# Kernel tuning notes

Hardware: AMD Instinct MI355X
Metric: run time of the kernel (lower is better)

Reference implementation:

```python
import jax, jax.numpy as jnp
import numpy as np
import math

D = 1024
H = 16

def _new_gelu(x):
    return 0.5 * x * (1.0 + jnp.tanh(math.sqrt(2.0 / math.pi) * (x + 0.044715 * x ** 3)))

def _layer_norm(x, w):
    mu = jnp.mean(x, axis=-1, keepdims=True)
    var = jnp.var(x, axis=-1, keepdims=True)
    return (x - mu) * jax.lax.rsqrt(var + 1e-5) * w

def setup_inputs() -> dict:
    key = jax.random.key(0)
    ks = jax.random.split(key, 8)
    B, T = 2, 2048
    s = lambda fan_in: 1.0 / math.sqrt(fan_in)
    return {
        "x": jax.random.normal(ks[0], (B, T, D), jnp.float32),
        "ln1_w": jnp.ones((D,), jnp.float32),
        "attn_w": jax.random.normal(ks[1], (D, 3 * D), jnp.float32) * s(D),
        "attn_b": jnp.zeros((3 * D,), jnp.float32),
        "proj_w": jax.random.normal(ks[2], (D, D), jnp.float32) * s(D),
        "proj_b": jnp.zeros((D,), jnp.float32),
        "ln2_w": jnp.ones((D,), jnp.float32),
        "li1_w": jax.random.normal(ks[3], (D, 4 * D), jnp.float32) * s(D),
        "li1_b": jnp.zeros((4 * D,), jnp.float32),
        "li2_w": jax.random.normal(ks[4], (4 * D, D), jnp.float32) * s(4 * D),
        "li2_b": jnp.zeros((D,), jnp.float32),
    }

def reference(x, ln1_w, attn_w, attn_b, proj_w, proj_b, ln2_w, li1_w, li1_b, li2_w, li2_b):
    B, T, C = x.shape
    Dh = C // H
    # --- causal self-attention on pre-LN input ---
    h = _layer_norm(x, ln1_w)
    qkv = h @ attn_w + attn_b                      # [B,T,3C]
    q, k, v = jnp.split(qkv, 3, axis=-1)
    q = q.reshape(B, T, H, Dh)
    k = k.reshape(B, T, H, Dh)
    v = v.reshape(B, T, H, Dh)
    # NOTE: faithful to source — scale is 1/sqrt(BATCH), not 1/sqrt(head_dim)
    scale = 1.0 / math.sqrt(B)
    scores = jnp.einsum('bthd,bshd->bhts', q, k) * scale   # [B,H,T,T]
    causal = jnp.tril(jnp.ones((T, T), bool))
    scores = jnp.where(causal, scores, -jnp.inf)
    attn = jax.nn.softmax(scores, axis=-1)
    o = jnp.einsum('bhts,bshd->bthd', attn, v).reshape(B, T, C)
    x = x + o @ proj_w + proj_b
    # --- MLP ---
    h = _layer_norm(x, ln2_w)
    x = x + _new_gelu(h @ li1_w + li1_b) @ li2_w + li2_b
    return x
```

## Files before the change

kernel.cpp:

```cpp
#include <hip/hip_runtime.h>

typedef _Float16 f16;
typedef _Float16 f16x8 __attribute__((ext_vector_type(8)));
typedef _Float16 f16x4 __attribute__((ext_vector_type(4)));
typedef float    f32x4 __attribute__((ext_vector_type(4)));
typedef float    f32x16 __attribute__((ext_vector_type(16)));
typedef unsigned u32;
typedef unsigned u32x4 __attribute__((ext_vector_type(4)));

#define GAS __attribute__((address_space(1)))
#define LAS __attribute__((address_space(3)))

static __device__ __forceinline__ void gload_lds16(const void* g, void* l) {
    __builtin_amdgcn_global_load_lds((const GAS void*)g, (LAS void*)l, 16, 0, 0);
}

__global__ void wconv_t(const float* __restrict__ w, f16* __restrict__ wt, int K, int N) {
    __shared__ f16 t[32][33];
    const int tx = threadIdx.x, ty = threadIdx.y;
    const int n0 = blockIdx.x * 32, k0 = blockIdx.y * 32;
#pragma unroll
    for (int i = 0; i < 4; i++)
        t[ty + i * 8][tx] = (f16)w[(size_t)(k0 + ty + i * 8) * N + n0 + tx];
    __syncthreads();
#pragma unroll
    for (int i = 0; i < 4; i++)
        wt[(size_t)(n0 + ty + i * 8) * K + k0 + tx] = t[tx][ty + i * 8];
}

__global__ __launch_bounds__(256) void ln_kernel(const float* __restrict__ x,
                                                 const float* __restrict__ w,
                                                 f16* __restrict__ h) {
    const int row = blockIdx.x, tid = threadIdx.x;
    const float4 v = reinterpret_cast<const float4*>(x)[(size_t)row * 256 + tid];
    float s = v.x + v.y + v.z + v.w;
    float q = v.x * v.x + v.y * v.y + v.z * v.z + v.w * v.w;
#pragma unroll
    for (int m = 1; m < 64; m <<= 1) { s += __shfl_xor(s, m); q += __shfl_xor(q, m); }
    __shared__ float ss[4], qq[4];
    if ((tid & 63) == 0) { ss[tid >> 6] = s; qq[tid >> 6] = q; }
    __syncthreads();
    s = ss[0] + ss[1] + ss[2] + ss[3];
    q = qq[0] + qq[1] + qq[2] + qq[3];
    const float mu = s * (1.0f / 1024.0f);
    const float var = q * (1.0f / 1024.0f) - mu * mu;
    const float rs = rsqrtf(var + 1e-5f);
    const float4 wv = reinterpret_cast<const float4*>(w)[tid];
    f16x4 o;
    o[0] = (f16)((v.x - mu) * rs * wv.x);
    o[1] = (f16)((v.y - mu) * rs * wv.y);
    o[2] = (f16)((v.z - mu) * rs * wv.z);
    o[3] = (f16)((v.w - mu) * rs * wv.w);
    reinterpret_cast<f16x4*>(h)[(size_t)row * 256 + tid] = o;
}

__global__ __launch_bounds__(256) void vtrans(const f16* __restrict__ V, f16* __restrict__ Vt) {
    __shared__ f16 tl[64][72];
    const int tid = threadIdx.x;
    const int t0 = blockIdx.x * 64, bh = blockIdx.y;
    const int b = bh >> 4, hh = bh & 15;
    const int rr = tid >> 3, cc = (tid & 7) * 8;
#pragma unroll
    for (int p = 0; p < 2; p++) {
        f16x8 v = *(const f16x8*)(V + (size_t)(b * 2048 + t0 + p * 32 + rr) * 1024 + hh * 64 + cc);
#pragma unroll
        for (int j = 0; j < 8; j++) tl[p * 32 + rr][cc + j] = v[j];
    }
    __syncthreads();
#pragma unroll
    for (int p = 0; p < 2; p++) {
        const int d = p * 32 + rr;
        f16x8 o;
#pragma unroll
        for (int j = 0; j < 8; j++) o[j] = tl[cc + j][d];
        *(f16x8*)(Vt + (size_t)(bh * 64 + d) * 2048 + t0 + cc) = o;
    }
}

template <int EPI>
__global__ __launch_bounds__(512) void gemm_f16(
    const f16* __restrict__ A, int lda,
    const f16* __restrict__ Bt, int ldb,
    const float* __restrict__ bias,
    const float* __restrict__ res,
    void* __restrict__ outp,
    f16* __restrict__ oq, f16* __restrict__ ok, f16* __restrict__ ov,
    int N, int K) {
    __shared__ alignas(16) f16 As[3][128 * 32];
    __shared__ alignas(16) f16 Bs[3][128 * 32];
    const int tid = threadIdx.x;
    const int lane = tid & 63, wv = tid >> 6;
    const int wr = wv >> 2, wc = wv & 3;
    const int m0 = blockIdx.x * 128, n0 = blockIdx.y * 128;
    const int l15 = lane & 15, lg = lane >> 4;

    f32x4 acc[4][2] = {};

    const int ar = tid >> 2;
    const int ac = (tid & 3) * 8;
    const size_t koff = (size_t)blockIdx.z * K;
    const f16* gA = A + (size_t)(m0 + ar) * lda + ac + koff;
    const f16* gB = Bt + (size_t)(n0 + ar) * ldb + ac + koff;
    char* lA0 = (char*)As + wv * 1024;
    char* lB0 = (char*)Bs + wv * 1024;

    auto stage = [&](int buf, int k0) {
        gload_lds16(gA + k0, lA0 + buf * 8192);
        gload_lds16(gB + k0, lB0 + buf * 8192);
    };
    auto compute = [&](int buf) {
        f16x8 af[4], bf[2];
#pragma unroll
        for (int i = 0; i < 4; i++)
            af[i] = *(const f16x8*)&As[buf][(wr * 64 + i * 16 + l15) * 32 + lg * 8];
#pragma unroll
        for (int n = 0; n < 2; n++)
            bf[n] = *(const f16x8*)&Bs[buf][(wc * 32 + n * 16 + l15) * 32 + lg * 8];
#pragma unroll
        for (int mi = 0; mi < 4; mi++)
#pragma unroll
            for (int ni = 0; ni < 2; ni++)
                acc[mi][ni] = __builtin_amdgcn_mfma_f32_16x16x32_f16(af[mi], bf[ni], acc[mi][ni], 0, 0, 0);
    };

    const int nk = K >> 5;
    stage(0, 0);
    if (nk > 1) {
        stage(1, 32);
        asm volatile("s_waitcnt vmcnt(2)" ::: "memory");
    } else {
        asm volatile("s_waitcnt vmcnt(0)" ::: "memory");
    }
    __builtin_amdgcn_s_barrier();

    for (int t = 0; t < nk; ++t) {
        const bool pref = (t + 2 < nk);
        if (pref) stage((t + 2) % 3, (t + 2) * 32);
        compute(t % 3);
        if (t + 1 < nk) {
            if (pref) asm volatile("s_waitcnt vmcnt(2)" ::: "memory");
            else      asm volatile("s_waitcnt vmcnt(0)" ::: "memory");
            __builtin_amdgcn_s_barrier();
        }
    }

#pragma unroll
    for (int mi = 0; mi < 4; mi++) {
#pragma unroll
        for (int ni = 0; ni < 2; ni++) {
            const int gc = n0 + wc * 32 + ni * 16 + l15;
            const float bb = (EPI == 3) ? 0.0f : bias[gc];
#pragma unroll
            for (int r = 0; r < 4; r++) {
                const int gr = m0 + wr * 64 + mi * 16 + lg * 4 + r;
                float v = acc[mi][ni][r] + bb;
                if (EPI == 0) {
                    if (gc < 1024)      oq[(size_t)gr * 1024 + gc]        = (f16)(v * 0.70710678118654752f);
                    else if (gc < 2048) ok[(size_t)gr * 1024 + gc - 1024] = (f16)v;
                    else                ov[(size_t)gr * 1024 + gc - 2048] = (f16)v;
                } else if (EPI == 1) {
                    ((float*)outp)[(size_t)gr * N + gc] = v + res[(size_t)gr * N + gc];
                } else if (EPI == 2) {
                    const float z = 0.7978845608028654f * (v + 0.044715f * v * v * v);
                    const float t = 1.0f - 2.0f / (__builtin_amdgcn_exp2f(2.8853900817779268f * z) + 1.0f);
                    ((f16*)outp)[(size_t)gr * N + gc] = (f16)(0.5f * v * (1.0f + t));
                } else {
                    float* P = (float*)outp + (size_t)blockIdx.z * ((size_t)gridDim.x * 128) * N;
                    P[(size_t)gr * N + gc] = v;
                }
            }
        }
    }
}

__global__ __launch_bounds__(256) void kred(const float* __restrict__ p0,
                                            const float* __restrict__ p1,
                                            const float* __restrict__ bias,
                                            const float* __restrict__ res,
                                            float* __restrict__ out) {
    const size_t i = (size_t)blockIdx.x * 256 + threadIdx.x;
    const float4 a = ((const float4*)p0)[i];
    const float4 b = ((const float4*)p1)[i];
    const float4 r = ((const float4*)res)[i];
    const float4 w = ((const float4*)bias)[i & 255];
    float4 o;
    o.x = a.x + b.x + r.x + w.x;
    o.y = a.y + b.y + r.y + w.y;
    o.z = a.z + b.z + r.z + w.z;
    o.w = a.w + b.w + r.w + w.w;
    ((float4*)out)[i] = o;
}

__global__ __launch_bounds__(256, 2) void attn_kernel(
    const f16* __restrict__ Q, const f16* __restrict__ Kb,
    const f16* __restrict__ Vt, f16* __restrict__ O) {
    __shared__ f16 ot[4][32][72];
    const int tid = threadIdx.x, lane = tid & 63, w = tid >> 6;
    const int l31 = lane & 31, hi = lane >> 5;
    const int bx = blockIdx.x;
    const int bh = bx & 31, jj = bx >> 5;
    const int b = bh >> 4, hh = bh & 15;
    const int qtile = (15 - jj) * 4 + w;
    const int q0 = qtile * 32;

    const f16* qrow = Q + (size_t)(b * 2048 + q0 + l31) * 1024 + hh * 64 + hi * 8;
    f16x8 qf[4];
#pragma unroll
    for (int s = 0; s < 4; s++) qf[s] = *(const f16x8*)(qrow + s * 16);

    f32x16 oacc[2] = {};
    float m = -3e38f, l = 0.0f;

    const f16* kbase = Kb + (size_t)b * 2048 * 1024 + hh * 64 + hi * 8;
    const f16* vrow0 = Vt + (size_t)(bh * 64 + l31) * 2048 + hi * 8;
    const f16* vrow1 = vrow0 + (size_t)32 * 2048;

    const int nt = qtile + 1;

    f16x8 ka[4], va[4], kb2[4], vb2[4];
    auto loadKV = [&](int kt, f16x8* kf, f16x8* vf) {
        const f16* kr = kbase + (size_t)(kt * 32 + l31) * 1024;
#pragma unroll
        for (int s = 0; s < 4; s++) kf[s] = *(const f16x8*)(kr + s * 16);
        vf[0] = *(const f16x8*)(vrow0 + kt * 32);
        vf[1] = *(const f16x8*)(vrow0 + kt * 32 + 16);
        vf[2] = *(const f16x8*)(vrow1 + kt * 32);
        vf[3] = *(const f16x8*)(vrow1 + kt * 32 + 16);
    };

    auto tilestep = [&](const f16x8* kf, const f16x8* vf, bool diag) {
        f32x16 sacc = {};
        __builtin_amdgcn_s_setprio(1);
#pragma unroll
        for (int s = 0; s < 4; s++)
            sacc = __builtin_amdgcn_mfma_f32_32x32x16_f16(kf[s], qf[s], sacc, 0, 0, 0);
        __builtin_amdgcn_s_setprio(0);
        if (diag) {
#pragma unroll
            for (int r = 0; r < 16; r++) {
                const int key = (r & 3) + 8 * (r >> 2) + 4 * hi;
                sacc[r] = (key > l31) ? -3e38f : sacc[r];
            }
        }
        float t8[8];
#pragma unroll
        for (int i = 0; i < 8; i++) t8[i] = fmaxf(sacc[2 * i], sacc[2 * i + 1]);
#pragma unroll
        for (int i = 0; i < 4; i++) t8[i] = fmaxf(t8[i], t8[i + 4]);
        float tm = fmaxf(fmaxf(t8[0], t8[1]), fmaxf(t8[2], t8[3]));
        tm = fmaxf(tm, __shfl_xor(tm, 32));
        const bool up = tm > m + 8.0f;
        if (__any(up)) {
            const float mnew = up ? tm : m;
            const float alpha = __expf(m - mnew);
            m = mnew;
            l *= alpha;
#pragma unroll
            for (int r = 0; r < 16; r++) { oacc[0][r] *= alpha; oacc[1][r] *= alpha; }
        }
        const float mref = m * 1.44269504f;
        float p[16];
#pragma unroll
        for (int r = 0; r < 16; r++)
            p[r] = __builtin_amdgcn_exp2f(sacc[r] * 1.44269504f - mref);
        float s8[8];
#pragma unroll
        for (int i = 0; i < 8; i++) s8[i] = p[2 * i] + p[2 * i + 1];
#pragma unroll
        for (int i = 0; i < 4; i++) s8[i] = s8[i] + s8[i + 4];
        float psum = (s8[0] + s8[1]) + (s8[2] + s8[3]);
        psum += __shfl_xor(psum, 32);
        l += psum;

        u32 wd[8];
#pragma unroll
        for (int i = 0; i < 8; i++)
            wd[i] = __builtin_bit_cast(u32, __builtin_amdgcn_cvt_pkrtz(p[2 * i], p[2 * i + 1]));
        const u32 e0 = __shfl_xor(hi ? wd[0] : wd[2], 32);
        const u32 e1 = __shfl_xor(hi ? wd[1] : wd[3], 32);
        const u32 e2 = __shfl_xor(hi ? wd[4] : wd[6], 32);
        const u32 e3 = __shfl_xor(hi ? wd[5] : wd[7], 32);
        u32x4 b0, b1;
        b0[0] = hi ? e0 : wd[0]; b0[1] = hi ? e1 : wd[1];
        b0[2] = hi ? wd[2] : e0; b0[3] = hi ? wd[3] : e1;
        b1[0] = hi ? e2 : wd[4]; b1[1] = hi ? e3 : wd[5];
        b1[2] = hi ? wd[6] : e2; b1[3] = hi ? wd[7] : e3;
        const f16x8 pb0 = __builtin_bit_cast(f16x8, b0);
        const f16x8 pb1 = __builtin_bit_cast(f16x8, b1);

        __builtin_amdgcn_s_setprio(1);
        oacc[0] = __builtin_amdgcn_mfma_f32_32x32x16_f16(vf[0], pb0, oacc[0], 0, 0, 0);
        oacc[0] = __builtin_amdgcn_mfma_f32_32x32x16_f16(vf[1], pb1, oacc[0], 0, 0, 0);
        oacc[1] = __builtin_amdgcn_mfma_f32_32x32x16_f16(vf[2], pb0, oacc[1], 0, 0, 0);
        oacc[1] = __builtin_amdgcn_mfma_f32_32x32x16_f16(vf[3], pb1, oacc[1], 0, 0, 0);
        __builtin_amdgcn_s_setprio(0);
    };

    loadKV(0, ka, va);
    int kt = 0;
    for (; kt + 2 <= nt; kt += 2) {
        loadKV(kt + 1, kb2, vb2);
        tilestep(ka, va, false);
        if (kt + 2 < nt) loadKV(kt + 2, ka, va);
        tilestep(kb2, vb2, (kt + 1) == qtile);
    }
    if (kt < nt) tilestep(ka, va, true);

    const float inv = 1.0f / l;
#pragma unroll
    for (int dt = 0; dt < 2; dt++)
#pragma unroll
        for (int r = 0; r < 16; r++) {
            const int d = dt * 32 + (r & 3) + 8 * (r >> 2) + 4 * hi;
            ot[w][l31][d] = (f16)(oacc[dt][r] * inv);
        }
    asm volatile("s_waitcnt lgkmcnt(0)" ::: "memory");
#pragma unroll
    for (int i = 0; i < 4; i++) {
        const int row = i * 8 + (lane >> 3), col = (lane & 7) * 8;
        const f16x8 o8 = *(const f16x8*)&ot[w][row][col];
        *(f16x8*)(O + (size_t)(b * 2048 + q0 + row) * 1024 + hh * 64 + col) = o8;
    }
}

extern "C" void kernel_launch(void* const* d_in, const int* in_sizes, int n_in,
                              void* d_out, int out_size, void* d_ws, size_t ws_size,
                              hipStream_t stream) {
    const float* x      = (const float*)d_in[0];
    const float* ln1_w  = (const float*)d_in[1];
    const float* attn_w = (const float*)d_in[2];
    const float* attn_b = (const float*)d_in[3];
    const float* proj_w = (const float*)d_in[4];
    const float* proj_b = (const float*)d_in[5];
    const float* ln2_w  = (const float*)d_in[6];
    const float* li1_w  = (const float*)d_in[7];
    const float* li1_b  = (const float*)d_in[8];
    const float* li2_w  = (const float*)d_in[9];
    const float* li2_b  = (const float*)d_in[10];
    float* out = (float*)d_out;

    char* ws = (char*)d_ws;
    size_t off = 0;
    auto alloc = [&](size_t bytes) { void* p = ws + off; off += (bytes + 255) & ~(size_t)255; return p; };
    f16* W1t = (f16*)alloc((size_t)3072 * 1024 * 2);
    f16* W2t = (f16*)alloc((size_t)1024 * 1024 * 2);
    f16* W3t = (f16*)alloc((size_t)4096 * 1024 * 2);
    f16* W4t = (f16*)alloc((size_t)1024 * 4096 * 2);
    f16* h   = (f16*)alloc((size_t)4096 * 1024 * 2);
    f16* Qb  = (f16*)alloc((size_t)4096 * 1024 * 2);
    f16* Kb  = (f16*)alloc((size_t)4096 * 1024 * 2);
    f16* Vb  = (f16*)alloc((size_t)4096 * 1024 * 2);
    f16* Vt  = (f16*)alloc((size_t)4096 * 1024 * 2);
    f16* Ob  = (f16*)alloc((size_t)4096 * 1024 * 2);
    float* x1 = (float*)alloc((size_t)4096 * 1024 * 4);
    float* P  = (float*)alloc((size_t)2 * 4096 * 1024 * 4);
    f16* Ab = Qb;

    dim3 b328(32, 8);
    wconv_t<<<dim3(96, 32),  b328, 0, stream>>>(attn_w, W1t, 1024, 3072);
    wconv_t<<<dim3(32, 32),  b328, 0, stream>>>(proj_w, W2t, 1024, 1024);
    wconv_t<<<dim3(128, 32), b328, 0, stream>>>(li1_w,  W3t, 1024, 4096);
    wconv_t<<<dim3(32, 128), b328, 0, stream>>>(li2_w,  W4t, 4096, 1024);

    ln_kernel<<<4096, 256, 0, stream>>>(x, ln1_w, h);
    gemm_f16<0><<<dim3(32, 24), 512, 0, stream>>>(h, 1024, W1t, 1024, attn_b, nullptr,
                                                  nullptr, Qb, Kb, Vb, 3072, 1024);
    vtrans<<<dim3(32, 32), 256, 0, stream>>>(Vb, Vt);
    attn_kernel<<<512, 256, 0, stream>>>(Qb, Kb, Vt, Ob);
    gemm_f16<1><<<dim3(32, 8), 512, 0, stream>>>(Ob, 1024, W2t, 1024, proj_b, x,
                                                 x1, nullptr, nullptr, nullptr, 1024, 1024);
    ln_kernel<<<4096, 256, 0, stream>>>(x1, ln2_w, h);
    gemm_f16<2><<<dim3(32, 32), 512, 0, stream>>>(h, 1024, W3t, 1024, li1_b, nullptr,
                                                  Ab, nullptr, nullptr, nullptr, 4096, 1024);
    gemm_f16<3><<<dim3(32, 8, 2), 512, 0, stream>>>(Ab, 4096, W4t, 4096, nullptr, nullptr,
                                                    P, nullptr, nullptr, nullptr, 1024, 2048);
    kred<<<4096, 256, 0, stream>>>(P, P + (size_t)4096 * 1024, li2_b, x1, out);
}
```

Measured before the change: 298.6 us.

## Split attention KV range across wave pairs with split-K softmax merge

Each block now handles two query tiles, a light one and its mirrored heavy one, using two waves per tile. The two waves split the causal KV range in half, and their partial softmax states are merged through shared memory. The grid doubles to 1024 blocks. The aim is to balance the causal workload and shorten the longest serial KV loop per wave. The cost is extra LDS traffic, a block-wide sync, and merge arithmetic.

```diff
diff --git a/kernel.cpp b/kernel.cpp
--- a/kernel.cpp
+++ b/kernel.cpp
@@ -194,14 +194,20 @@
 __global__ __launch_bounds__(256, 2) void attn_kernel(
     const f16* __restrict__ Q, const f16* __restrict__ Kb,
     const f16* __restrict__ Vt, f16* __restrict__ O) {
-    __shared__ f16 ot[4][32][72];
+    __shared__ float ob[2][64][33];
+    __shared__ float mlb[2][2][64];
+    __shared__ f16 ot[2][32][72];
     const int tid = threadIdx.x, lane = tid & 63, w = tid >> 6;
     const int l31 = lane & 31, hi = lane >> 5;
     const int bx = blockIdx.x;
-    const int bh = bx & 31, jj = bx >> 5;
+    const int bh = bx & 31, g = bx >> 5;
     const int b = bh >> 4, hh = bh & 15;
-    const int qtile = (15 - jj) * 4 + w;
+    const int qtile = (w < 2) ? g : 63 - g;
     const int q0 = qtile * 32;
+    const int nt = qtile + 1;
+    const int hsplit = (nt + 1) >> 1;
+    const int k0 = (w & 1) ? hsplit : 0;
+    const int k1 = (w & 1) ? nt : hsplit;
 
     const f16* qrow = Q + (size_t)(b * 2048 + q0 + l31) * 1024 + hh * 64 + hi * 8;
     f16x8 qf[4];
@@ -214,8 +220,6 @@
     const f16* kbase = Kb + (size_t)b * 2048 * 1024 + hh * 64 + hi * 8;
     const f16* vrow0 = Vt + (size_t)(bh * 64 + l31) * 2048 + hi * 8;
     const f16* vrow1 = vrow0 + (size_t)32 * 2048;
-
-    const int nt = qtile + 1;
 
     f16x8 ka[4], va[4], kb2[4], vb2[4];
     auto loadKV = [&](int kt, f16x8* kf, f16x8* vf) {
@@ -296,30 +300,51 @@
         __builtin_amdgcn_s_setprio(0);
     };
 
-    loadKV(0, ka, va);
-    int kt = 0;
-    for (; kt + 2 <= nt; kt += 2) {
-        loadKV(kt + 1, kb2, vb2);
-        tilestep(ka, va, false);
-        if (kt + 2 < nt) loadKV(kt + 2, ka, va);
-        tilestep(kb2, vb2, (kt + 1) == qtile);
-    }
-    if (kt < nt) tilestep(ka, va, true);
-
-    const float inv = 1.0f / l;
-#pragma unroll
-    for (int dt = 0; dt < 2; dt++)
-#pragma unroll
-        for (int r = 0; r < 16; r++) {
-            const int d = dt * 32 + (r & 3) + 8 * (r >> 2) + 4 * hi;
-            ot[w][l31][d] = (f16)(oacc[dt][r] * inv);
-        }
-    asm volatile("s_waitcnt lgkmcnt(0)" ::: "memory");
-#pragma unroll
-    for (int i = 0; i < 4; i++) {
-        const int row = i * 8 + (lane >> 3), col = (lane & 7) * 8;
-        const f16x8 o8 = *(const f16x8*)&ot[w][row][col];
-        *(f16x8*)(O + (size_t)(b * 2048 + q0 + row) * 1024 + hh * 64 + col) = o8;
+    if (k0 < k1) {
+        loadKV(k0, ka, va);
+        int kt = k0;
+        for (; kt + 2 <= k1; kt += 2) {
+            loadKV(kt + 1, kb2, vb2);
+            tilestep(ka, va, kt == qtile);
+            if (kt + 2 < k1) loadKV(kt + 2, ka, va);
+            tilestep(kb2, vb2, (kt + 1) == qtile);
+        }
+        if (kt < k1) tilestep(ka, va, kt == qtile);
+    }
+
+    const int pair = w >> 1;
+    if (!(w & 1)) {
+#pragma unroll
+        for (int dt = 0; dt < 2; dt++)
+#pragma unroll
+            for (int r = 0; r < 16; r++)
+                ob[pair][lane][dt * 16 + r] = oacc[dt][r];
+        mlb[pair][0][lane] = m;
+        mlb[pair][1][lane] = l;
+    }
+    __syncthreads();
+    if (w & 1) {
+        const float m1 = mlb[pair][0][lane];
+        const float l1 = mlb[pair][1][lane];
+        const float ms = fmaxf(m, m1);
+        const float a0 = __expf(m - ms);
+        const float a1 = __expf(m1 - ms);
+        const float inv = 1.0f / (l * a0 + l1 * a1);
+#pragma unroll
+        for (int dt = 0; dt < 2; dt++)
+#pragma unroll
+            for (int r = 0; r < 16; r++) {
+                const int d = dt * 32 + (r & 3) + 8 * (r >> 2) + 4 * hi;
+                const float val = (oacc[dt][r] * a0 + ob[pair][lane][dt * 16 + r] * a1) * inv;
+                ot[pair][l31][d] = (f16)val;
+            }
+        asm volatile("s_waitcnt lgkmcnt(0)" ::: "memory");
+#pragma unroll
+        for (int i = 0; i < 4; i++) {
+            const int row = i * 8 + (lane >> 3), col = (lane & 7) * 8;
+            const f16x8 o8 = *(const f16x8*)&ot[pair][row][col];
+            *(f16x8*)(O + (size_t)(b * 2048 + q0 + row) * 1024 + hh * 64 + col) = o8;
+        }
     }
 }
 
@@ -366,7 +391,7 @@
     gemm_f16<0><<<dim3(32, 24), 512, 0, stream>>>(h, 1024, W1t, 1024, attn_b, nullptr,
                                                   nullptr, Qb, Kb, Vb, 3072, 1024);
     vtrans<<<dim3(32, 32), 256, 0, stream>>>(Vb, Vt);
-    attn_kernel<<<512, 256, 0, stream>>>(Qb, Kb, Vt, Ob);
+    attn_kernel<<<1024, 256, 0, stream>>>(Qb, Kb, Vt, Ob);
     gemm_f16<1><<<dim3(32, 8), 512, 0, stream>>>(Ob, 1024, W2t, 1024, proj_b, x,
                                                  x1, nullptr, nullptr, nullptr, 1024, 1024);
     ln_kernel<<<4096, 256, 0, stream>>>(x1, ln2_w, h);
```

Result: faster. 277.6 us (-7.0%).

## Stage K/V tiles through swizzled LDS with triple-buffered async loads in attention

Applied to the files above, without the earlier changes.

The attention kernel no longer has each wave load its own K/V fragments from global memory into registers. K and V tiles are now shared by all four waves of a block, brought into a triple-buffered, XOR-swizzled LDS pool with global_load_lds and synchronised by vmcnt waits and barriers. Query blocks are assigned in an interleaved heavy/light order to balance the causal workload, and the launch_bounds occupancy hint is dropped. The goal is to cut redundant global/L2 traffic, since four waves previously fetched the same keys, at the cost of block-wide barriers that make waves wait for the slowest one.

```diff
diff --git a/kernel.cpp b/kernel.cpp
--- a/kernel.cpp
+++ b/kernel.cpp
@@ -191,17 +191,20 @@
     ((float4*)out)[i] = o;
 }
 
-__global__ __launch_bounds__(256, 2) void attn_kernel(
+__global__ __launch_bounds__(256) void attn_kernel(
     const f16* __restrict__ Q, const f16* __restrict__ Kb,
     const f16* __restrict__ Vt, f16* __restrict__ O) {
-    __shared__ f16 ot[4][32][72];
+    __shared__ alignas(16) char pool[24576];
     const int tid = threadIdx.x, lane = tid & 63, w = tid >> 6;
     const int l31 = lane & 31, hi = lane >> 5;
     const int bx = blockIdx.x;
-    const int bh = bx & 31, jj = bx >> 5;
+    const int j = bx >> 5, bh = bx & 31;
+    const int qb = (j < 8) ? (15 - 2 * j) : (2 * (j - 8));
     const int b = bh >> 4, hh = bh & 15;
-    const int qtile = (15 - jj) * 4 + w;
+    const int qtile = qb * 4 + w;
     const int q0 = qtile * 32;
+    const int ntw = qtile + 1;
+    const int nk = qb * 4 + 4;
 
     const f16* qrow = Q + (size_t)(b * 2048 + q0 + l31) * 1024 + hh * 64 + hi * 8;
     f16x8 qf[4];
@@ -211,24 +214,33 @@
     f32x16 oacc[2] = {};
     float m = -3e38f, l = 0.0f;
 
-    const f16* kbase = Kb + (size_t)b * 2048 * 1024 + hh * 64 + hi * 8;
-    const f16* vrow0 = Vt + (size_t)(bh * 64 + l31) * 2048 + hi * 8;
-    const f16* vrow1 = vrow0 + (size_t)32 * 2048;
-
-    const int nt = qtile + 1;
-
-    f16x8 ka[4], va[4], kb2[4], vb2[4];
-    auto loadKV = [&](int kt, f16x8* kf, f16x8* vf) {
-        const f16* kr = kbase + (size_t)(kt * 32 + l31) * 1024;
-#pragma unroll
-        for (int s = 0; s < 4; s++) kf[s] = *(const f16x8*)(kr + s * 16);
-        vf[0] = *(const f16x8*)(vrow0 + kt * 32);
-        vf[1] = *(const f16x8*)(vrow0 + kt * 32 + 16);
-        vf[2] = *(const f16x8*)(vrow1 + kt * 32);
-        vf[3] = *(const f16x8*)(vrow1 + kt * 32 + 16);
+    const f16* kg = Kb + (size_t)b * 2048 * 1024 + (size_t)(tid >> 3) * 1024 + hh * 64
+                    + ((tid & 7) ^ ((tid >> 3) & 7)) * 8;
+    const f16* vg = Vt + (size_t)(bh * 64 + (tid >> 2)) * 2048
+                    + (((tid & 3) ^ ((tid >> 3) & 3)) * 8);
+    char* kld = pool + tid * 16;
+    char* vld = pool + 4096 + tid * 16;
+
+    auto stage = [&](int buf, int kt) {
+        gload_lds16(kg + (size_t)kt * 32768, kld + buf * 8192);
+        gload_lds16(vg + kt * 32, vld + buf * 8192);
     };
 
-    auto tilestep = [&](const f16x8* kf, const f16x8* vf, bool diag) {
+    const int ksw = (l31 & 7);
+    const int vsw = ((l31 >> 1) & 3);
+
+    auto tilestep = [&](int buf, bool diag) {
+        const f16* Kbuf = (const f16*)(pool + buf * 8192);
+        const f16* Vbuf = (const f16*)(pool + buf * 8192 + 4096);
+        f16x8 kf[4], vf[4];
+#pragma unroll
+        for (int si = 0; si < 4; si++)
+            kf[si] = *(const f16x8*)&Kbuf[l31 * 64 + (((si * 2 + hi) ^ ksw) * 8)];
+        vf[0] = *(const f16x8*)&Vbuf[l31 * 32 + ((hi ^ vsw) * 8)];
+        vf[1] = *(const f16x8*)&Vbuf[l31 * 32 + (((2 + hi) ^ vsw) * 8)];
+        vf[2] = *(const f16x8*)&Vbuf[(32 + l31) * 32 + ((hi ^ vsw) * 8)];
+        vf[3] = *(const f16x8*)&Vbuf[(32 + l31) * 32 + (((2 + hi) ^ vsw) * 8)];
+
         f32x16 sacc = {};
         __builtin_amdgcn_s_setprio(1);
 #pragma unroll
@@ -296,29 +308,36 @@
         __builtin_amdgcn_s_setprio(0);
     };
 
-    loadKV(0, ka, va);
-    int kt = 0;
-    for (; kt + 2 <= nt; kt += 2) {
-        loadKV(kt + 1, kb2, vb2);
-        tilestep(ka, va, false);
-        if (kt + 2 < nt) loadKV(kt + 2, ka, va);
-        tilestep(kb2, vb2, (kt + 1) == qtile);
-    }
-    if (kt < nt) tilestep(ka, va, true);
-
+    stage(0, 0);
+    stage(1, 1);
+    asm volatile("s_waitcnt vmcnt(2)" ::: "memory");
+    __builtin_amdgcn_s_barrier();
+    for (int t = 0; t < nk; ++t) {
+        const bool pref = (t + 2 < nk);
+        if (pref) stage((t + 2) % 3, t + 2);
+        if (t < ntw) tilestep(t % 3, t == qtile);
+        if (t + 1 < nk) {
+            if (pref) asm volatile("s_waitcnt vmcnt(2)" ::: "memory");
+            else      asm volatile("s_waitcnt vmcnt(0)" ::: "memory");
+            __builtin_amdgcn_s_barrier();
+        }
+    }
+
+    __syncthreads();
+    f16* otw = (f16*)(pool) + w * (32 * 72);
     const float inv = 1.0f / l;
 #pragma unroll
     for (int dt = 0; dt < 2; dt++)
 #pragma unroll
         for (int r = 0; r < 16; r++) {
             const int d = dt * 32 + (r & 3) + 8 * (r >> 2) + 4 * hi;
-            ot[w][l31][d] = (f16)(oacc[dt][r] * inv);
+            otw[l31 * 72 + d] = (f16)(oacc[dt][r] * inv);
         }
     asm volatile("s_waitcnt lgkmcnt(0)" ::: "memory");
 #pragma unroll
     for (int i = 0; i < 4; i++) {
         const int row = i * 8 + (lane >> 3), col = (lane & 7) * 8;
-        const f16x8 o8 = *(const f16x8*)&ot[w][row][col];
+        const f16x8 o8 = *(const f16x8*)&otw[row * 72 + col];
         *(f16x8*)(O + (size_t)(b * 2048 + q0 + row) * 1024 + hh * 64 + col) = o8;
     }
 }
```

Measured after the change: 277.8 us. 7.0% less time.
